# Kernel optimization log

Hardware: AMD Instinct MI355X
Metric: run time of the kernel (lower is better)

The kernel has to match this reference:

```python
import jax, jax.numpy as jnp
import numpy as np

N_NODES = 50000
N_EDGES = 800000
N_GRAPHS = 128
D_IN, D_HID, D_OUT = 128, 128, 128  # gnn_input_dim, gnn_hidden_dim, gnn_output_dim
EPS = 1e-5
NEG_SLOPE = 0.01


def setup_inputs() -> dict:
    key = jax.random.key(0)
    ks = jax.random.split(key, 16)
    x = jax.random.normal(ks[0], (N_NODES, D_IN), jnp.float32)
    edge_index = jax.random.randint(ks[1], (2, N_EDGES), 0, N_NODES, dtype=jnp.int64)
    batch = jnp.sort(jax.random.randint(ks[2], (N_NODES,), 0, N_GRAPHS, dtype=jnp.int64))

    def lin(k, fi, fo):
        return jax.random.normal(k, (fi, fo), jnp.float32) * (1.0 / np.sqrt(fi))

    d2, d4 = 2 * D_HID, 4 * D_HID
    return {
        "x": x, "edge_index": edge_index, "batch": batch, "batch_size": N_GRAPHS,
        "W1": lin(ks[3], D_IN, d2), "b1": jnp.zeros((d2,), jnp.float32),
        "g1": jnp.ones((d2,), jnp.float32), "be1": jnp.zeros((d2,), jnp.float32),
        "W2": lin(ks[4], d2, d4), "b2": jnp.zeros((d4,), jnp.float32),
        "g2": jnp.ones((d4,), jnp.float32), "be2": jnp.zeros((d4,), jnp.float32),
        "W3": lin(ks[5], d4, d4), "b3": jnp.zeros((d4,), jnp.float32),
        "g3": jnp.ones((d4,), jnp.float32), "be3": jnp.zeros((d4,), jnp.float32),
        "Wf": lin(ks[6], d4, D_OUT), "bf": jnp.zeros((D_OUT,), jnp.float32),
    }


def _layernorm(h, g, b):
    mu = jnp.mean(h, axis=-1, keepdims=True)
    var = jnp.mean(jnp.square(h - mu), axis=-1, keepdims=True)
    return (h - mu) * jax.lax.rsqrt(var + EPS) * g + b


def _gcn_conv(h, W, b, src, dst, norm, n):
    # h' = D^-1/2 (A+I) D^-1/2 (h W) + b   (PyG GCNConv with self-loops)
    m = h @ W                                    # [N, F_out]
    msg = m[src] * norm[:, None]                 # [E+N, F_out]
    return jax.ops.segment_sum(msg, dst, num_segments=n) + b


def reference(x, edge_index, batch, batch_size, W1, b1, g1, be1,
              W2, b2, g2, be2, W3, b3, g3, be3, Wf, bf):
    n = x.shape[0]
    loop = jnp.arange(n, dtype=edge_index.dtype)
    src = jnp.concatenate([edge_index[0], loop])
    dst = jnp.concatenate([edge_index[1], loop])
    deg = jax.ops.segment_sum(jnp.ones_like(dst, dtype=x.dtype), dst, num_segments=n)
    dinv = jax.lax.rsqrt(deg)                    # deg >= 1 due to self loops
    norm = dinv[src] * dinv[dst]

    h = _gcn_conv(x, W1, b1, src, dst, norm, n)
    h = jax.nn.leaky_relu(_layernorm(h, g1, be1), NEG_SLOPE)
    h = _gcn_conv(h, W2, b2, src, dst, norm, n)
    h = jax.nn.leaky_relu(_layernorm(h, g2, be2), NEG_SLOPE)
    h = _gcn_conv(h, W3, b3, src, dst, norm, n)
    h = _layernorm(h, g3, be3)

    # global average pool per graph
    sums = jax.ops.segment_sum(h, batch, num_segments=batch_size)
    cnt = jax.ops.segment_sum(jnp.ones((n,), h.dtype), batch, num_segments=batch_size)
    pooled = sums / jnp.maximum(cnt, 1.0)[:, None]
    return pooled @ Wf + bf
```

## Files before the change

kernel.cpp:

```cpp
#include <hip/hip_runtime.h>
#include <hip/hip_bf16.h>
#include <math.h>

#define GRAPHS 128
#define SCAN_B 256
#define BM 128
#define BN 128
#define PCH 128
#define WSCALE 2097152.0f

typedef __attribute__((ext_vector_type(4))) int i32x4;

__device__ inline unsigned short f2b(float f) {
    unsigned int u = __float_as_uint(f);
    unsigned int r = (u + 0x7fffu + ((u >> 16) & 1u)) >> 16;
    return (unsigned short)r;
}
__device__ inline float b2f(unsigned short u) {
    return __uint_as_float(((unsigned int)u) << 16);
}
__device__ inline void unpack8(float* v, uint4 u) {
    v[0] = b2f(u.x & 0xffffu); v[1] = b2f(u.x >> 16);
    v[2] = b2f(u.y & 0xffffu); v[3] = b2f(u.y >> 16);
    v[4] = b2f(u.z & 0xffffu); v[5] = b2f(u.z >> 16);
    v[6] = b2f(u.w & 0xffffu); v[7] = b2f(u.w >> 16);
}

__device__ inline void gload16(const void* g, void* l) {
    typedef unsigned int __attribute__((address_space(1))) gu32;
    typedef unsigned int __attribute__((address_space(3))) su32;
    __builtin_amdgcn_global_load_lds((const gu32*)g, (su32*)l, 16, 0, 0);
}

__device__ inline int xcd_vid(int p, int nwg) {
    int q = nwg >> 3, r = nwg & 7, x = p & 7, ix = p >> 3;
    return (x < r ? x * (q + 1) : r * (q + 1) + (x - r) * q) + ix;
}


__global__ void k_count(const int* __restrict__ dst, int* __restrict__ cnt, int E) {
    int i = blockIdx.x * blockDim.x + threadIdx.x;
    if (i < E) atomicAdd(&cnt[dst[i]], 1);
}

__global__ void k_scan1(const int* __restrict__ cnt, int* __restrict__ excl,
                        int* __restrict__ bsum, int n) {
    __shared__ int sh[SCAN_B];
    int t = threadIdx.x;
    int i = blockIdx.x * SCAN_B + t;
    int v = (i < n) ? cnt[i] : 0;
    sh[t] = v;
    __syncthreads();
    for (int off = 1; off < SCAN_B; off <<= 1) {
        int x = (t >= off) ? sh[t - off] : 0;
        __syncthreads();
        sh[t] += x;
        __syncthreads();
    }
    if (i < n) excl[i] = sh[t] - v;
    if (t == SCAN_B - 1) bsum[blockIdx.x] = sh[t];
}

__global__ void k_scan2(int* __restrict__ bsum, int nb) {
    __shared__ int sh[SCAN_B];
    int t = threadIdx.x;
    int v = (t < nb) ? bsum[t] : 0;
    sh[t] = v;
    __syncthreads();
    for (int off = 1; off < SCAN_B; off <<= 1) {
        int x = (t >= off) ? sh[t - off] : 0;
        __syncthreads();
        sh[t] += x;
        __syncthreads();
    }
    if (t < nb) bsum[t] = sh[t] - v;
}

__global__ void k_scan3(int* __restrict__ rowstart, const int* __restrict__ bsum,
                        const int* __restrict__ cnt, float* __restrict__ dinv,
                        int* __restrict__ cursor, int n, int E) {
    int i = blockIdx.x * SCAN_B + threadIdx.x;
    if (i < n) {
        rowstart[i] += bsum[blockIdx.x];
        cursor[i] = 0;
        dinv[i] = rsqrtf((float)cnt[i] + 1.0f);
    }
    if (i == 0) rowstart[n] = E;
}

__global__ void k_scatter_csr(const int* __restrict__ src, const int* __restrict__ dst,
                              const float* __restrict__ dinv, const int* __restrict__ rowstart,
                              int* __restrict__ cursor, int2* __restrict__ csr, int E) {
    int e = blockIdx.x * blockDim.x + threadIdx.x;
    if (e >= E) return;
    int s = src[e], d = dst[e];
    int pos = rowstart[d] + atomicAdd(&cursor[d], 1);
    int2 c;
    c.x = s;
    c.y = __float_as_int(dinv[s] * dinv[d]);
    csr[pos] = c;
}


__global__ void k_prep(const float* __restrict__ W1, const float* __restrict__ W2,
                       const float* __restrict__ W3, signed char* __restrict__ T1,
                       signed char* __restrict__ T2, signed char* __restrict__ T3,
                       float* __restrict__ S1, float* __restrict__ S2,
                       float* __restrict__ S3, const float* __restrict__ x,
                       signed char* __restrict__ qx, float* __restrict__ sx,
                       const float* __restrict__ g1, const float* __restrict__ be1,
                       const float* __restrict__ g2, const float* __restrict__ be2,
                       float* __restrict__ scf, float* __restrict__ scfi,
                       int n, int mpad, int nblk) {
    int lane = threadIdx.x & 63;
    if ((int)blockIdx.x == nblk - 1) {
        int w = threadIdx.x >> 6;
        if (w < 2) {
            const float* g = w ? g2 : g1;
            const float* be = w ? be2 : be1;
            int nn = w ? 512 : 256;
            float mg = 0.f, mb = 0.f;
            for (int i = lane; i < nn; i += 64) {
                mg = fmaxf(mg, fabsf(g[i]));
                mb = fmaxf(mb, fabsf(be[i]));
            }
#pragma unroll
            for (int m = 1; m < 64; m <<= 1) {
                mg = fmaxf(mg, __shfl_xor(mg, m));
                mb = fmaxf(mb, __shfl_xor(mb, m));
            }
            if (lane == 0) {
                float s = (6.0f * mg + mb) * (1.0f / 127.0f);
                scf[w] = s;
                scfi[w] = 1.0f / s;
            }
        }
        return;
    }
    if (blockIdx.x < 320) {
        int w = blockIdx.x * 4 + (threadIdx.x >> 6);
        const float* W; signed char* T; float* S; int K, N, col;
        if (w < 256) { W = W1; T = T1; S = S1; K = 128; N = 256; col = w; }
        else if (w < 768) { W = W2; T = T2; S = S2; K = 256; N = 512; col = w - 256; }
        else { W = W3; T = T3; S = S3; K = 512; N = 512; col = w - 768; }
        int epl = K >> 6;
        float v[8];
        float mx = 0.f;
        for (int j = 0; j < epl; ++j) {
            float xx = W[(size_t)(lane * epl + j) * N + col];
            v[j] = xx;
            mx = fmaxf(mx, fabsf(xx));
        }
#pragma unroll
        for (int m = 1; m < 64; m <<= 1) mx = fmaxf(mx, __shfl_xor(mx, m));
        float inv = (mx > 0.f) ? 127.0f / mx : 0.f;
        signed char* tp = T + (size_t)col * K + lane * epl;
        for (int j = 0; j < epl; ++j) tp[j] = (signed char)__float2int_rn(v[j] * inv);
        if (lane == 0) S[col] = mx * (1.0f / 127.0f);
        return;
    }
    int row = (blockIdx.x - 320) * 4 + (threadIdx.x >> 6);
    if (row >= mpad) return;
    signed char* qp = qx + (size_t)row * 128 + lane * 2;
    if (row >= n) {
        *(unsigned short*)qp = 0;
        if (lane == 0) sx[row] = 0.f;
        return;
    }
    float2 v = *(const float2*)(x + (size_t)row * 128 + lane * 2);
    float mx = fmaxf(fabsf(v.x), fabsf(v.y));
#pragma unroll
    for (int m = 1; m < 64; m <<= 1) mx = fmaxf(mx, __shfl_xor(mx, m));
    float inv = (mx > 0.f) ? 127.0f / mx : 0.f;
    int q0 = __float2int_rn(v.x * inv), q1 = __float2int_rn(v.y * inv);
    *(unsigned short*)qp = (unsigned short)((q0 & 0xff) | ((q1 & 0xff) << 8));
    if (lane == 0) sx[row] = mx * (1.0f / 127.0f);
}


__device__ inline void accw(int* a, unsigned int u, int wq) {
    a[0] += __mul24((int)(signed char)(u), wq);
    a[1] += __mul24((int)(signed char)(u >> 8), wq);
    a[2] += __mul24((int)(signed char)(u >> 16), wq);
    a[3] += __mul24((int)(signed char)(u >> 24), wq);
}
__device__ inline void acc16(int* a, uint4 u, int wq) {
    accw(a, u.x, wq);
    accw(a + 4, u.y, wq);
    accw(a + 8, u.z, wq);
    accw(a + 12, u.w, wq);
}

template <int F, bool FIXS>
__global__ void k_agg8(const signed char* __restrict__ q8, const float* __restrict__ scale,
                       const float* __restrict__ scf, int li,
                       signed char* __restrict__ qa, float* __restrict__ sa,
                       const int* __restrict__ rowstart, const int2* __restrict__ csr,
                       const float* __restrict__ dinv, int n, int mpad) {
    constexpr int TPN = F / 16;
    constexpr int NPB = 256 / TPN;
    int node = blockIdx.x * NPB + (int)(threadIdx.x / TPN);
    int sub = (int)(threadIdx.x % TPN);
    int fo = sub * 16;
    if (node >= mpad) return;
    signed char* outp = qa + (size_t)node * F + fo;
    if (node >= n) {
        uint4 z = {0u, 0u, 0u, 0u};
        *(uint4*)outp = z;
        if (sub == 0) sa[node] = 0.f;
        return;
    }

    float kconst = FIXS ? scf[li] * WSCALE : 0.f;
    const signed char* qf = q8 + fo;
    float di = dinv[node];
    int a[16] = {};
    {
        uint4 u = *(const uint4*)(qf + (size_t)node * F);
        float ws = FIXS ? di * di * kconst : di * di * scale[node] * WSCALE;
        acc16(a, u, __float2int_rn(ws));
    }
    int b = rowstart[node], e = rowstart[node + 1];
    int j = b;
    for (; j + 2 <= e; j += 2) {
        int2 c0 = csr[j], c1 = csr[j + 1];
        uint4 u0 = *(const uint4*)(qf + (size_t)c0.x * F);
        uint4 u1 = *(const uint4*)(qf + (size_t)c1.x * F);
        int w0, w1;
        if (FIXS) {
            w0 = __float2int_rn(__int_as_float(c0.y) * kconst);
            w1 = __float2int_rn(__int_as_float(c1.y) * kconst);
        } else {
            w0 = __float2int_rn(__int_as_float(c0.y) * scale[c0.x] * WSCALE);
            w1 = __float2int_rn(__int_as_float(c1.y) * scale[c1.x] * WSCALE);
        }
        acc16(a, u0, w0);
        acc16(a, u1, w1);
    }
    for (; j < e; ++j) {
        int2 c = csr[j];
        uint4 u = *(const uint4*)(qf + (size_t)c.x * F);
        int wq = FIXS ? __float2int_rn(__int_as_float(c.y) * kconst)
                      : __float2int_rn(__int_as_float(c.y) * scale[c.x] * WSCALE);
        acc16(a, u, wq);
    }
    int amax = 0;
#pragma unroll
    for (int k = 0; k < 16; ++k) amax = max(amax, abs(a[k]));
#pragma unroll
    for (int m = 1; m < TPN; m <<= 1) amax = max(amax, __shfl_xor(amax, m));

    float inv = (amax > 0) ? 127.0f / (float)amax : 0.f;
    unsigned int ob[4];
#pragma unroll
    for (int wi = 0; wi < 4; ++wi) {
        unsigned int o = 0;
#pragma unroll
        for (int k = 0; k < 4; ++k)
            o |= ((unsigned)(__float2int_rn((float)a[wi * 4 + k] * inv) & 0xff)) << (8 * k);
        ob[wi] = o;
    }
    *(uint4*)outp = *(uint4*)ob;
    if (sub == 0) sa[node] = (float)amax * (1.0f / (127.0f * WSCALE));
}


__global__ __launch_bounds__(256) void k_gemm_i8(
    const signed char* __restrict__ A, const float* __restrict__ srow,
    const signed char* __restrict__ BT, const float* __restrict__ scol,
    const float* __restrict__ bias, unsigned short* __restrict__ C,
    int K, int N, int ncb) {
    __shared__ __align__(16) char sA[BM * 128];
    __shared__ __align__(16) char sB[BN * 128];

    const int vid = xcd_vid((int)blockIdx.x, (int)gridDim.x);
    const int rb = vid / ncb;
    const int cb = vid - rb * ncb;
    const int tid = threadIdx.x;
    const int lane = tid & 63;
    const int wave = tid >> 6;
    const int wr = wave >> 1, wc = wave & 1;
    const size_t row0 = (size_t)rb * BM;
    const size_t col0 = (size_t)cb * BN;

    const signed char* srcA[4];
    const signed char* srcB[4];
    char* dstA[4];
    char* dstB[4];
#pragma unroll
    for (int c = 0; c < 4; ++c) {
        int idx = c * 256 + tid;
        int row = idx >> 3;
        int cbl = ((idx & 7) << 4) ^ ((row & 7) << 4);
        srcA[c] = A + (row0 + row) * K + cbl;
        srcB[c] = BT + (col0 + row) * K + cbl;
        dstA[c] = sA + idx * 16;
        dstB[c] = sB + idx * 16;
    }

    const int fr = lane & 15;
    const int fg = lane >> 4;
    const int fsw = (lane & 7) << 4;
    int offA[4][2], offB[4][2];
#pragma unroll
    for (int t = 0; t < 4; ++t)
#pragma unroll
        for (int kk = 0; kk < 2; ++kk) {
            offA[t][kk] = (wr * 64 + t * 16 + fr) * 128 + ((kk * 64 + fg * 16) ^ fsw);
            offB[t][kk] = (wc * 64 + t * 16 + fr) * 128 + ((kk * 64 + fg * 16) ^ fsw);
        }

    i32x4 acc[4][4] = {};

    for (int k0 = 0; k0 < K; k0 += 128) {
#pragma unroll
        for (int c = 0; c < 4; ++c) gload16(srcA[c] + k0, dstA[c]);
#pragma unroll
        for (int c = 0; c < 4; ++c) gload16(srcB[c] + k0, dstB[c]);
        __syncthreads();
#pragma unroll
        for (int kk = 0; kk < 2; ++kk) {
            i32x4 av[4], bv[4];
#pragma unroll
            for (int t = 0; t < 4; ++t) av[t] = *(const i32x4*)(sA + offA[t][kk]);
#pragma unroll
            for (int t = 0; t < 4; ++t) bv[t] = *(const i32x4*)(sB + offB[t][kk]);
#pragma unroll
            for (int i = 0; i < 4; ++i)
#pragma unroll
                for (int j = 0; j < 4; ++j)
                    acc[i][j] = __builtin_amdgcn_mfma_i32_16x16x64_i8(av[i], bv[j],
                                                                      acc[i][j], 0, 0, 0);
        }
        __syncthreads();
    }

    float sr[4][4];
#pragma unroll
    for (int i = 0; i < 4; ++i)
#pragma unroll
        for (int q = 0; q < 4; ++q)
            sr[i][q] = srow[row0 + wr * 64 + i * 16 + fg * 4 + q];

#pragma unroll
    for (int i = 0; i < 4; ++i) {
#pragma unroll
        for (int j = 0; j < 4; ++j) {
            size_t r = row0 + wr * 64 + i * 16 + fg * 4;
            size_t cc = col0 + wc * 64 + j * 16 + fr;
            float scc = scol[cc];
            float bb = bias[cc];
#pragma unroll
            for (int q = 0; q < 4; ++q)
                C[(r + q) * N + cc] = f2b((float)acc[i][j][q] * (sr[i][q] * scc) + bb);
        }
    }
}


template <int F, bool LRELU>
__global__ void k_lnq(const unsigned short* __restrict__ z, signed char* __restrict__ q8,
                      const float* __restrict__ scfi, int li,
                      const float* __restrict__ g, const float* __restrict__ be, int mpad) {
    constexpr int V = F / 64;
    int row = blockIdx.x * 4 + (threadIdx.x >> 6);
    int lane = threadIdx.x & 63;
    const unsigned short* p = z + (size_t)row * F + lane * V;
    float v[V];
    if constexpr (V == 8) {
        uint4 u = *(const uint4*)p;
        unpack8(v, u);
    } else {
        uint2 u = *(const uint2*)p;
        v[0] = b2f(u.x & 0xffffu); v[1] = b2f(u.x >> 16);
        v[2] = b2f(u.y & 0xffffu); v[3] = b2f(u.y >> 16);
    }
    float s = 0.f, q = 0.f;
#pragma unroll
    for (int k = 0; k < V; ++k) { s += v[k]; q += v[k] * v[k]; }
#pragma unroll
    for (int m = 1; m < 64; m <<= 1) {
        s += __shfl_xor(s, m);
        q += __shfl_xor(q, m);
    }
    float mu = s * (1.0f / F);
    float var = q * (1.0f / F) - mu * mu;
    float rs = rsqrtf(var + 1e-5f);
    float inv = scfi[li];

    unsigned int ob[V / 4];
#pragma unroll
    for (int k = 0; k < V; k += 4) {
        unsigned int o = 0;
#pragma unroll
        for (int t = 0; t < 4; ++t) {
            float yy = (v[k + t] - mu) * rs * g[lane * V + k + t] + be[lane * V + k + t];
            if (LRELU) yy = fmaxf(yy, 0.f) + 0.01f * fminf(yy, 0.f);
            int qi = __float2int_rn(yy * inv);
            qi = min(127, max(-127, qi));
            o |= ((unsigned)(qi & 0xff)) << (8 * t);
        }
        ob[k / 4] = o;
    }
    signed char* qp = q8 + (size_t)row * F + lane * V;
    if constexpr (V == 8) *(uint2*)qp = *(uint2*)ob;
    else                  *(unsigned int*)qp = ob[0];
}


__global__ void k_pool4(const unsigned short* __restrict__ z, const float* __restrict__ g,
                        const float* __restrict__ be, const int* __restrict__ batch,
                        float* __restrict__ pooled, int n) {
    int i0 = blockIdx.x * PCH;
    int iend = i0 + PCH; if (iend > n) iend = n;
    int w = threadIdx.x >> 6, lane = threadIdx.x & 63;
    int f0 = lane * 8;
    float gk[8], ek[8];
    {
        float4 ga = *(const float4*)(g + f0), gb = *(const float4*)(g + f0 + 4);
        float4 ea = *(const float4*)(be + f0), eb = *(const float4*)(be + f0 + 4);
        gk[0] = ga.x; gk[1] = ga.y; gk[2] = ga.z; gk[3] = ga.w;
        gk[4] = gb.x; gk[5] = gb.y; gk[6] = gb.z; gk[7] = gb.w;
        ek[0] = ea.x; ek[1] = ea.y; ek[2] = ea.z; ek[3] = ea.w;
        ek[4] = eb.x; ek[5] = eb.y; ek[6] = eb.z; ek[7] = eb.w;
    }
    float a[8] = {};
    int cur = -1;
    for (int i = i0 + w; i < iend; i += 4) {
        int gg = batch[i];
        if (gg != cur) {
            if (cur >= 0) {
                float* pp = pooled + (size_t)cur * 512 + f0;
#pragma unroll
                for (int k = 0; k < 8; ++k) atomicAdd(&pp[k], a[k]);
            }
#pragma unroll
            for (int k = 0; k < 8; ++k) a[k] = 0.f;
            cur = gg;
        }
        uint4 u = *(const uint4*)(z + (size_t)i * 512 + f0);
        float v[8]; unpack8(v, u);
        float s = 0.f, q = 0.f;
#pragma unroll
        for (int k = 0; k < 8; ++k) { s += v[k]; q += v[k] * v[k]; }
#pragma unroll
        for (int m = 1; m < 64; m <<= 1) {
            s += __shfl_xor(s, m);
            q += __shfl_xor(q, m);
        }
        float mu = s * (1.0f / 512.0f);
        float var = q * (1.0f / 512.0f) - mu * mu;
        float rs = rsqrtf(var + 1e-5f);
#pragma unroll
        for (int k = 0; k < 8; ++k) a[k] += (v[k] - mu) * rs * gk[k] + ek[k];
    }
    if (cur >= 0) {
        float* pp = pooled + (size_t)cur * 512 + f0;
#pragma unroll
        for (int k = 0; k < 8; ++k) atomicAdd(&pp[k], a[k]);
    }
}


__global__ void k_final(const float* __restrict__ pooled, const int* __restrict__ batch,
                        const float* __restrict__ Wf, const float* __restrict__ bf,
                        float* __restrict__ out, int n) {
    int gph = blockIdx.x;
    int o = threadIdx.x;
    int lo = 0, hi = n;
    while (lo < hi) { int mid = (lo + hi) >> 1; if (batch[mid] < gph) lo = mid + 1; else hi = mid; }
    int start = lo;
    lo = start; hi = n;
    while (lo < hi) { int mid = (lo + hi) >> 1; if (batch[mid] < gph + 1) lo = mid + 1; else hi = mid; }
    int end = lo;
    float inv = 1.0f / fmaxf((float)(end - start), 1.0f);

    __shared__ float p[512];
    for (int k = threadIdx.x; k < 512; k += 128) p[k] = pooled[(size_t)gph * 512 + k] * inv;
    __syncthreads();
    float acc = bf[o];
#pragma unroll 8
    for (int k = 0; k < 512; ++k) acc += p[k] * Wf[(size_t)k * 128 + o];
    out[(size_t)gph * 128 + o] = acc;
}


static inline size_t align_up(size_t x) { return (x + 255) & ~(size_t)255; }

extern "C" void kernel_launch(void* const* d_in, const int* in_sizes, int n_in,
                              void* d_out, int out_size, void* d_ws, size_t ws_size,
                              hipStream_t stream) {
    const float* x     = (const float*)d_in[0];
    const int*   ei    = (const int*)d_in[1];
    const int*   batch = (const int*)d_in[2];
    const float* W1 = (const float*)d_in[4],  *b1 = (const float*)d_in[5];
    const float* g1 = (const float*)d_in[6],  *be1= (const float*)d_in[7];
    const float* W2 = (const float*)d_in[8],  *b2 = (const float*)d_in[9];
    const float* g2 = (const float*)d_in[10], *be2= (const float*)d_in[11];
    const float* W3 = (const float*)d_in[12], *b3 = (const float*)d_in[13];
    const float* g3 = (const float*)d_in[14], *be3= (const float*)d_in[15];
    const float* Wf = (const float*)d_in[16], *bf = (const float*)d_in[17];
    float* out = (float*)d_out;

    const int N = in_sizes[0] / 128;
    const int E = in_sizes[1] / 2;
    const int Mpad = ((N + BM - 1) / BM) * BM;
    const int* src = ei;
    const int* dst = ei + E;

    char* ws = (char*)d_ws;
    size_t off = 0;
    auto take = [&](size_t bytes) { char* p = ws + off; off += align_up(bytes); return p; };

    int*            cnt     = (int*)  take((size_t)N * 4);
    float*          pooled  = (float*)take((size_t)GRAPHS * 512 * 4);
    unsigned short* zb      = (unsigned short*)take((size_t)Mpad * 512 * 2);
    signed char*    qa      = (signed char*)take((size_t)Mpad * 512);
    float*          sa      = (float*)take((size_t)Mpad * 4);
    signed char*    q8      = (signed char*)take((size_t)Mpad * 512);
    signed char*    q8x     = (signed char*)take((size_t)Mpad * 128);
    float*          sx      = (float*)take((size_t)Mpad * 4);
    signed char*    wq1     = (signed char*)take((size_t)256 * 128);
    signed char*    wq2     = (signed char*)take((size_t)512 * 256);
    signed char*    wq3     = (signed char*)take((size_t)512 * 512);
    float*          sc1     = (float*)take(256 * 4);
    float*          sc2     = (float*)take(512 * 4);
    float*          sc3     = (float*)take(512 * 4);
    float*          scf     = (float*)take(2 * 4);
    float*          scfi    = (float*)take(2 * 4);
    float*          dinv    = (float*)take((size_t)N * 4);
    int*            rowstart= (int*)  take((size_t)(N + 1) * 4);
    int*            cursor  = (int*)  take((size_t)N * 4);
    int*            bsum    = (int*)  take((size_t)SCAN_B * 4);
    int2*           csr     = (int2*) take((size_t)E * 8);

    const int nb = (N + SCAN_B - 1) / SCAN_B;
    const int NR4 = Mpad / 4;
    const int nprep = 320 + NR4 + 1;

    hipMemsetAsync(cnt, 0, (size_t)((char*)(pooled + GRAPHS * 512) - (char*)cnt), stream);

    k_count<<<(E + 255) / 256, 256, 0, stream>>>(dst, cnt, E);
    k_scan1<<<nb, SCAN_B, 0, stream>>>(cnt, rowstart, bsum, N);
    k_scan2<<<1, SCAN_B, 0, stream>>>(bsum, nb);
    k_scan3<<<nb, SCAN_B, 0, stream>>>(rowstart, bsum, cnt, dinv, cursor, N, E);
    k_scatter_csr<<<(E + 255) / 256, 256, 0, stream>>>(src, dst, dinv, rowstart, cursor, csr, E);

    k_prep<<<nprep, 256, 0, stream>>>(W1, W2, W3, wq1, wq2, wq3, sc1, sc2, sc3,
                                      x, q8x, sx, g1, be1, g2, be2, scf, scfi, N, Mpad, nprep);

    k_agg8<128, false><<<Mpad / 32, 256, 0, stream>>>(q8x, sx, nullptr, 0, qa, sa,
                                                      rowstart, csr, dinv, N, Mpad);
    k_gemm_i8<<<(Mpad / BM) * 2, 256, 0, stream>>>(qa, sa, wq1, sc1, b1, zb, 128, 256, 2);
    k_lnq<256, true><<<NR4, 256, 0, stream>>>(zb, q8, scfi, 0, g1, be1, Mpad);

    k_agg8<256, true><<<Mpad / 16, 256, 0, stream>>>(q8, nullptr, scf, 0, qa, sa,
                                                     rowstart, csr, dinv, N, Mpad);
    k_gemm_i8<<<(Mpad / BM) * 4, 256, 0, stream>>>(qa, sa, wq2, sc2, b2, zb, 256, 512, 4);
    k_lnq<512, true><<<NR4, 256, 0, stream>>>(zb, q8, scfi, 1, g2, be2, Mpad);

    k_agg8<512, true><<<Mpad / 8, 256, 0, stream>>>(q8, nullptr, scf, 1, qa, sa,
                                                    rowstart, csr, dinv, N, Mpad);
    k_gemm_i8<<<(Mpad / BM) * 4, 256, 0, stream>>>(qa, sa, wq3, sc3, b3, zb, 512, 512, 4);

    k_pool4<<<(N + PCH - 1) / PCH, 256, 0, stream>>>(zb, g3, be3, batch, pooled, N);
    k_final<<<GRAPHS, 128, 0, stream>>>(pooled, batch, Wf, bf, out, N);
}
```

Measured before the change: 389.0 us.

## Fuse CSR scan into one block and merge scatter with prep kernel

Replaces the three-kernel block scan with a single 1024-thread kernel that scans per-thread chunks serially, and merges the CSR scatter and the weight/input quantization prep into one launch. CSR edge weights are now stored as pre-scaled fixed-point integers, so the aggregation inner loop uses them directly. The per-layer LayerNorm scale is applied once to the output row scale instead of per edge. This cuts kernel launches and per-edge float-to-int conversions. The cost is a serial single-block scan over 50k counts and possibly different rounding of the quantized weights.

```diff
diff --git a/kernel.cpp b/kernel.cpp
--- a/kernel.cpp
+++ b/kernel.cpp
@@ -43,102 +43,67 @@
     if (i < E) atomicAdd(&cnt[dst[i]], 1);
 }
 
-__global__ void k_scan1(const int* __restrict__ cnt, int* __restrict__ excl,
-                        int* __restrict__ bsum, int n) {
-    __shared__ int sh[SCAN_B];
+__global__ __launch_bounds__(1024) void k_scan_all(const int* __restrict__ cnt,
+                                                   int* __restrict__ rowstart,
+                                                   float* __restrict__ dinv,
+                                                   int* __restrict__ cursor, int n, int E) {
+    __shared__ int sh[1024];
     int t = threadIdx.x;
-    int i = blockIdx.x * SCAN_B + t;
-    int v = (i < n) ? cnt[i] : 0;
-    sh[t] = v;
+    const int per = (n + 1023) / 1024;
+    int i0 = t * per;
+    int i1 = i0 + per; if (i1 > n) i1 = n;
+    int s = 0;
+    for (int i = i0; i < i1; ++i) s += cnt[i];
+    sh[t] = s;
     __syncthreads();
-    for (int off = 1; off < SCAN_B; off <<= 1) {
-        int x = (t >= off) ? sh[t - off] : 0;
+    for (int off = 1; off < 1024; off <<= 1) {
+        int v = (t >= off) ? sh[t - off] : 0;
         __syncthreads();
-        sh[t] += x;
+        sh[t] += v;
         __syncthreads();
     }
-    if (i < n) excl[i] = sh[t] - v;
-    if (t == SCAN_B - 1) bsum[blockIdx.x] = sh[t];
-}
-
-__global__ void k_scan2(int* __restrict__ bsum, int nb) {
-    __shared__ int sh[SCAN_B];
-    int t = threadIdx.x;
-    int v = (t < nb) ? bsum[t] : 0;
-    sh[t] = v;
-    __syncthreads();
-    for (int off = 1; off < SCAN_B; off <<= 1) {
-        int x = (t >= off) ? sh[t - off] : 0;
-        __syncthreads();
-        sh[t] += x;
-        __syncthreads();
-    }
-    if (t < nb) bsum[t] = sh[t] - v;
-}
-
-__global__ void k_scan3(int* __restrict__ rowstart, const int* __restrict__ bsum,
-                        const int* __restrict__ cnt, float* __restrict__ dinv,
-                        int* __restrict__ cursor, int n, int E) {
-    int i = blockIdx.x * SCAN_B + threadIdx.x;
-    if (i < n) {
-        rowstart[i] += bsum[blockIdx.x];
+    int base = (t > 0) ? sh[t - 1] : 0;
+    for (int i = i0; i < i1; ++i) {
+        int c = cnt[i];
+        rowstart[i] = base;
         cursor[i] = 0;
-        dinv[i] = rsqrtf((float)cnt[i] + 1.0f);
-    }
-    if (i == 0) rowstart[n] = E;
-}
-
-__global__ void k_scatter_csr(const int* __restrict__ src, const int* __restrict__ dst,
-                              const float* __restrict__ dinv, const int* __restrict__ rowstart,
-                              int* __restrict__ cursor, int2* __restrict__ csr, int E) {
-    int e = blockIdx.x * blockDim.x + threadIdx.x;
-    if (e >= E) return;
-    int s = src[e], d = dst[e];
-    int pos = rowstart[d] + atomicAdd(&cursor[d], 1);
-    int2 c;
-    c.x = s;
-    c.y = __float_as_int(dinv[s] * dinv[d]);
-    csr[pos] = c;
-}
-
-
-__global__ void k_prep(const float* __restrict__ W1, const float* __restrict__ W2,
-                       const float* __restrict__ W3, signed char* __restrict__ T1,
-                       signed char* __restrict__ T2, signed char* __restrict__ T3,
-                       float* __restrict__ S1, float* __restrict__ S2,
-                       float* __restrict__ S3, const float* __restrict__ x,
-                       signed char* __restrict__ qx, float* __restrict__ sx,
-                       const float* __restrict__ g1, const float* __restrict__ be1,
-                       const float* __restrict__ g2, const float* __restrict__ be2,
-                       float* __restrict__ scf, float* __restrict__ scfi,
-                       int n, int mpad, int nblk) {
+        dinv[i] = rsqrtf((float)c + 1.0f);
+        base += c;
+    }
+    if (t == 0) rowstart[n] = E;
+}
+
+
+__global__ void k_scatter_prep(
+    const int* __restrict__ src, const int* __restrict__ dst,
+    const float* __restrict__ dinv, const int* __restrict__ rowstart,
+    int* __restrict__ cursor, int2* __restrict__ csr, int E, int nscat,
+    const float* __restrict__ W1, const float* __restrict__ W2,
+    const float* __restrict__ W3, signed char* __restrict__ T1,
+    signed char* __restrict__ T2, signed char* __restrict__ T3,
+    float* __restrict__ S1, float* __restrict__ S2, float* __restrict__ S3,
+    const float* __restrict__ x, signed char* __restrict__ qx, float* __restrict__ sx,
+    const float* __restrict__ g1, const float* __restrict__ be1,
+    const float* __restrict__ g2, const float* __restrict__ be2,
+    float* __restrict__ scf, float* __restrict__ scfi,
+    int n, int mpad, int nblk) {
     int lane = threadIdx.x & 63;
-    if ((int)blockIdx.x == nblk - 1) {
-        int w = threadIdx.x >> 6;
-        if (w < 2) {
-            const float* g = w ? g2 : g1;
-            const float* be = w ? be2 : be1;
-            int nn = w ? 512 : 256;
-            float mg = 0.f, mb = 0.f;
-            for (int i = lane; i < nn; i += 64) {
-                mg = fmaxf(mg, fabsf(g[i]));
-                mb = fmaxf(mb, fabsf(be[i]));
-            }
-#pragma unroll
-            for (int m = 1; m < 64; m <<= 1) {
-                mg = fmaxf(mg, __shfl_xor(mg, m));
-                mb = fmaxf(mb, __shfl_xor(mb, m));
-            }
-            if (lane == 0) {
-                float s = (6.0f * mg + mb) * (1.0f / 127.0f);
-                scf[w] = s;
-                scfi[w] = 1.0f / s;
-            }
+    int b = (int)blockIdx.x;
+    if (b < nscat) {
+        int e = b * 256 + threadIdx.x;
+        if (e < E) {
+            int s = src[e], d = dst[e];
+            int pos = rowstart[d] + atomicAdd(&cursor[d], 1);
+            int2 c;
+            c.x = s;
+            c.y = __float2int_rn(dinv[s] * dinv[d] * WSCALE);
+            csr[pos] = c;
         }
         return;
     }
-    if (blockIdx.x < 320) {
-        int w = blockIdx.x * 4 + (threadIdx.x >> 6);
+    b -= nscat;
+    if (b < 320) {
+        int w = b * 4 + (threadIdx.x >> 6);
         const float* W; signed char* T; float* S; int K, N, col;
         if (w < 256) { W = W1; T = T1; S = S1; K = 128; N = 256; col = w; }
         else if (w < 768) { W = W2; T = T2; S = S2; K = 256; N = 512; col = w - 256; }
@@ -159,7 +124,32 @@
         if (lane == 0) S[col] = mx * (1.0f / 127.0f);
         return;
     }
-    int row = (blockIdx.x - 320) * 4 + (threadIdx.x >> 6);
+    b -= 320;
+    if (b == nblk - nscat - 321) {
+        int w = threadIdx.x >> 6;
+        if (w < 2) {
+            const float* g = w ? g2 : g1;
+            const float* be = w ? be2 : be1;
+            int nn = w ? 512 : 256;
+            float mg = 0.f, mb = 0.f;
+            for (int i = lane; i < nn; i += 64) {
+                mg = fmaxf(mg, fabsf(g[i]));
+                mb = fmaxf(mb, fabsf(be[i]));
+            }
+#pragma unroll
+            for (int m = 1; m < 64; m <<= 1) {
+                mg = fmaxf(mg, __shfl_xor(mg, m));
+                mb = fmaxf(mb, __shfl_xor(mb, m));
+            }
+            if (lane == 0) {
+                float s = (6.0f * mg + mb) * (1.0f / 127.0f);
+                scf[w] = s;
+                scfi[w] = 1.0f / s;
+            }
+        }
+        return;
+    }
+    int row = b * 4 + (threadIdx.x >> 6);
     if (row >= mpad) return;
     signed char* qp = qx + (size_t)row * 128 + lane * 2;
     if (row >= n) {
@@ -211,13 +201,12 @@
         return;
     }
 
-    float kconst = FIXS ? scf[li] * WSCALE : 0.f;
     const signed char* qf = q8 + fo;
     float di = dinv[node];
     int a[16] = {};
     {
         uint4 u = *(const uint4*)(qf + (size_t)node * F);
-        float ws = FIXS ? di * di * kconst : di * di * scale[node] * WSCALE;
+        float ws = FIXS ? di * di * WSCALE : di * di * scale[node] * WSCALE;
         acc16(a, u, __float2int_rn(ws));
     }
     int b = rowstart[node], e = rowstart[node + 1];
@@ -228,11 +217,11 @@
         uint4 u1 = *(const uint4*)(qf + (size_t)c1.x * F);
         int w0, w1;
         if (FIXS) {
-            w0 = __float2int_rn(__int_as_float(c0.y) * kconst);
-            w1 = __float2int_rn(__int_as_float(c1.y) * kconst);
+            w0 = c0.y;
+            w1 = c1.y;
         } else {
-            w0 = __float2int_rn(__int_as_float(c0.y) * scale[c0.x] * WSCALE);
-            w1 = __float2int_rn(__int_as_float(c1.y) * scale[c1.x] * WSCALE);
+            w0 = __float2int_rn((float)c0.y * scale[c0.x]);
+            w1 = __float2int_rn((float)c1.y * scale[c1.x]);
         }
         acc16(a, u0, w0);
         acc16(a, u1, w1);
@@ -240,8 +229,7 @@
     for (; j < e; ++j) {
         int2 c = csr[j];
         uint4 u = *(const uint4*)(qf + (size_t)c.x * F);
-        int wq = FIXS ? __float2int_rn(__int_as_float(c.y) * kconst)
-                      : __float2int_rn(__int_as_float(c.y) * scale[c.x] * WSCALE);
+        int wq = FIXS ? c.y : __float2int_rn((float)c.y * scale[c.x]);
         acc16(a, u, wq);
     }
     int amax = 0;
@@ -261,7 +249,11 @@
         ob[wi] = o;
     }
     *(uint4*)outp = *(uint4*)ob;
-    if (sub == 0) sa[node] = (float)amax * (1.0f / (127.0f * WSCALE));
+    if (sub == 0) {
+        float s = (float)amax * (1.0f / (127.0f * WSCALE));
+        if (FIXS) s *= scf[li];
+        sa[node] = s;
+    }
 }
 
 
@@ -531,23 +523,20 @@
     float*          dinv    = (float*)take((size_t)N * 4);
     int*            rowstart= (int*)  take((size_t)(N + 1) * 4);
     int*            cursor  = (int*)  take((size_t)N * 4);
-    int*            bsum    = (int*)  take((size_t)SCAN_B * 4);
     int2*           csr     = (int2*) take((size_t)E * 8);
 
-    const int nb = (N + SCAN_B - 1) / SCAN_B;
     const int NR4 = Mpad / 4;
-    const int nprep = 320 + NR4 + 1;
+    const int SCAT = (E + 255) / 256;
+    const int nblk = SCAT + 320 + NR4 + 1;
 
     hipMemsetAsync(cnt, 0, (size_t)((char*)(pooled + GRAPHS * 512) - (char*)cnt), stream);
 
     k_count<<<(E + 255) / 256, 256, 0, stream>>>(dst, cnt, E);
-    k_scan1<<<nb, SCAN_B, 0, stream>>>(cnt, rowstart, bsum, N);
-    k_scan2<<<1, SCAN_B, 0, stream>>>(bsum, nb);
-    k_scan3<<<nb, SCAN_B, 0, stream>>>(rowstart, bsum, cnt, dinv, cursor, N, E);
-    k_scatter_csr<<<(E + 255) / 256, 256, 0, stream>>>(src, dst, dinv, rowstart, cursor, csr, E);
-
-    k_prep<<<nprep, 256, 0, stream>>>(W1, W2, W3, wq1, wq2, wq3, sc1, sc2, sc3,
-                                      x, q8x, sx, g1, be1, g2, be2, scf, scfi, N, Mpad, nprep);
+    k_scan_all<<<1, 1024, 0, stream>>>(cnt, rowstart, dinv, cursor, N, E);
+    k_scatter_prep<<<nblk, 256, 0, stream>>>(src, dst, dinv, rowstart, cursor, csr, E, SCAT,
+                                             W1, W2, W3, wq1, wq2, wq3, sc1, sc2, sc3,
+                                             x, q8x, sx, g1, be1, g2, be2, scf, scfi,
+                                             N, Mpad, nblk);
 
     k_agg8<128, false><<<Mpad / 32, 256, 0, stream>>>(q8x, sx, nullptr, 0, qa, sa,
                                                       rowstart, csr, dinv, N, Mpad);
```

New measurement: 508.6 us. 30.7% more time.
